# Optimization experiments

Hardware: AMD Instinct MI355X
Metric: run time of the kernel (lower is better)

The kernel has to match this reference:

```python
import jax, jax.numpy as jnp
import numpy as np

B, C, T = 8, 512, 8192
NQ, CBS, CBD = 9, 1024, 8
EPS = 1e-12  # F.normalize eps


def setup_inputs() -> dict:
    key = jax.random.key(0)
    ks = jax.random.split(key, 12)
    n = lambda i, shape, s: jax.random.normal(ks[i], shape, jnp.float32) * s
    return {
        "z": n(0, (B, C, T), 1.0),
        "down_w": n(1, (2, C, C, 2), 0.02),   # [layer, out, in, k] (torch Conv1d layout)
        "down_b": n(2, (2, C), 0.01),
        "up_w": n(3, (2, C, C, 2), 0.02),     # [layer, in, out, k] (torch ConvTranspose1d layout)
        "up_b": n(4, (2, C), 0.01),
        "in_v": n(5, (NQ, CBD, C), 0.05),     # weight_norm direction of in_proj 1x1 conv
        "in_g": 1.0 + n(6, (NQ, CBD), 0.02),  # weight_norm magnitude
        "in_b": n(7, (NQ, CBD), 0.01),
        "out_v": n(8, (NQ, C, CBD), 0.05),
        "out_g": 1.0 + n(9, (NQ, C), 0.02),
        "out_b": n(10, (NQ, C), 0.01),
        "codebooks": n(11, (NQ, CBS, CBD), 1.0),
    }


def _wn(g, v):
    # weight_norm (dim=0): per-output-row rescale
    return g[:, None] * v / jnp.linalg.norm(v, axis=1, keepdims=True)


def _l2norm(x):
    return x / jnp.maximum(jnp.linalg.norm(x, axis=-1, keepdims=True), EPS)


def _forward(z, down_w, down_b, up_w, up_b, in_v, in_g, in_b, out_v, out_g, out_b, codebooks):
    # --- downsample: two Conv1d(k=2, s=2) ---
    x = z
    for l in range(2):
        b, c, t = x.shape
        xr = x.reshape(b, c, t // 2, 2)
        x = jnp.einsum('bitk,oik->bot', xr, down_w[l]) + down_b[l][None, :, None]

    residual = x
    z_q = jnp.zeros_like(x)
    commit_loss = jnp.float32(0.0)
    cb_loss = jnp.float32(0.0)
    codes = []
    for i in range(NQ):
        # in_proj 1x1 conv (weight-normed)
        w_in = _wn(in_g[i], in_v[i])                 # [CBD, C]
        z_e = jnp.einsum('bdt,cd->bct', residual, w_in) + in_b[i][None, :, None]  # [B, CBD, T']
        # decode_latents: L2-normalize + squared-euclid via matmul + argmax
        bt = z_e.shape[0] * z_e.shape[2]
        enc = z_e.transpose(0, 2, 1).reshape(bt, CBD)
        enc_n = _l2norm(enc)
        cbk = codebooks[i]
        cb_n = _l2norm(cbk)
        dist = ((enc_n ** 2).sum(1, keepdims=True)
                - 2.0 * enc_n @ cb_n.T
                + (cb_n ** 2).sum(1)[None, :])        # [B*T', CBS]
        idx = jnp.argmax(-dist, axis=1).reshape(z_e.shape[0], -1)  # [B, T']
        z_q_i = cbk[idx].transpose(0, 2, 1)           # [B, CBD, T'] (un-normalized codebook rows)
        # losses (eval: mask all-true -> per-batch mean over (1,2) then batch mean == global mean)
        commit_loss = commit_loss + ((z_e - jax.lax.stop_gradient(z_q_i)) ** 2).mean()
        cb_loss = cb_loss + ((z_q_i - jax.lax.stop_gradient(z_e)) ** 2).mean()
        # straight-through + out_proj 1x1 conv (weight-normed)
        z_st = z_e + jax.lax.stop_gradient(z_q_i - z_e)
        w_out = _wn(out_g[i], out_v[i])               # [C, CBD]
        z_q_out = jnp.einsum('bct,dc->bdt', z_st, w_out) + out_b[i][None, :, None]
        z_q = z_q + z_q_out
        residual = residual - z_q_out
        codes.append(idx)
    codes = jnp.stack(codes, axis=1)                  # [B, NQ, T']

    x = z_q
    for l in range(2):
        b, c, t = x.shape
        x = jnp.einsum('bit,iok->botk', x, up_w[l]).reshape(b, C, t * 2) + up_b[l][None, :, None]
    return x, codes, commit_loss, cb_loss


def reference(z, down_w, down_b, up_w, up_b, in_v, in_g, in_b, out_v, out_g, out_b, codebooks):
    return _forward(z, down_w, down_b, up_w, up_b, in_v, in_g, in_b, out_v, out_g, out_b, codebooks)
```

## Files before the change

### kernel.cpp

```cpp
#include <hip/hip_runtime.h>
#include <math.h>


using u16 = unsigned short;
typedef __attribute__((ext_vector_type(8))) short bf16x8;
typedef __attribute__((ext_vector_type(8))) u16 su16x8;
typedef __attribute__((ext_vector_type(4))) float f32x4;

constexpr int NQ = 9, CBS = 1024, CBD = 8;
constexpr int TQ = 2048;
constexpr int NTOK = 16384;
constexpr int APS = 1048576;
#define EPSN 1e-12f

constexpr size_t OFF_X2    = 0;
constexpr size_t OFF_E0T   = 8388608;
constexpr size_t OFF_Q     = 9568256;
constexpr size_t OFF_WD    = 10747904;
constexpr size_t OFF_WDP   = 11796480;
constexpr size_t OFF_WEFF  = 13369344;
constexpr size_t OFF_WX    = 14417920;
constexpr size_t OFF_WINN  = 14581760;
constexpr size_t OFF_WOUTS = 14618624;
constexpr size_t OFF_CBS   = 14659584;
constexpr size_t OFF_PT    = 14678016;
constexpr size_t OFF_BEFF  = 14680356;
constexpr size_t OFF_BSUM  = 14680428;
constexpr size_t OFF_BD    = 14680940;
constexpr size_t OFF_BUP   = 14681452;
constexpr size_t OFF_LOSS  = 14682476;

__global__ void prep_small1(const float* __restrict__ in_v, const float* __restrict__ in_g,
                            const float* __restrict__ out_v, const float* __restrict__ out_g,
                            const float* __restrict__ out_b, const float* __restrict__ codebooks,
                            const float* __restrict__ down_w, const float* __restrict__ down_b,
                            const float* __restrict__ up_w, const float* __restrict__ up_b,
                            float* __restrict__ ws) {
  int bid = blockIdx.x, tid = threadIdx.x;
  int wid4 = tid >> 6, lane = tid & 63;
  if (bid < 18) {
    int wid = bid * 4 + wid4;
    if (wid < 72) {
      const float* v = in_v + (size_t)wid * 512;
      float ss = 0.f;
      for (int c = lane; c < 512; c += 64) ss += v[c] * v[c];
      #pragma unroll
      for (int o = 32; o; o >>= 1) ss += __shfl_xor(ss, o);
      float sc = in_g[wid] / sqrtf(ss);
      float* dst = ws + OFF_WINN + (size_t)wid * 512;
      for (int c = lane; c < 512; c += 64) dst[c] = v[c] * sc;
    }
  } else if (bid < 36) {
    int r = (bid - 18) * 256 + tid;
    if (r < 4608) {
      int i = r >> 9, c = r & 511;
      const float* v = out_v + (size_t)r * 8;
      float ss = 0.f;
      #pragma unroll
      for (int d = 0; d < 8; d++) ss += v[d] * v[d];
      float sc = out_g[r] / sqrtf(ss);
      float* dst = ws + OFF_WOUTS + (size_t)c * 80 + i * 8;
      #pragma unroll
      for (int d = 0; d < 8; d++) dst[d] = v[d] * sc;
    }
  } else if (bid < 72) {
    int r = (bid - 36) * 256 + tid;
    if (r < 9216) {
      int i = r >> 10, j = r & 1023;
      const float* v = codebooks + (size_t)r * 8;
      float ss = 0.f;
      #pragma unroll
      for (int d = 0; d < 8; d++) ss += v[d] * v[d];
      float nm = fmaxf(sqrtf(ss), EPSN);
      float nsq = 0.f;
      #pragma unroll
      for (int d = 0; d < 8; d++) { float cn = v[d] / nm; nsq += cn * cn; }
      ws[OFF_CBS + ((size_t)i * 2 + 0) * 1024 + j] = 2.0f / nm;
      ws[OFF_CBS + ((size_t)i * 2 + 1) * 1024 + j] = nsq;
    }
  } else if (bid < 74) {
    int c = (bid - 72) * 256 + tid;
    if (c < 512) {
      float s = 0.f;
      #pragma unroll
      for (int j = 0; j < 9; j++) s += out_b[j * 512 + c];
      ws[OFF_BSUM + c] = s;
      ws[OFF_WOUTS + (size_t)c * 80 + 72] = s;
      #pragma unroll
      for (int d = 73; d < 80; d++) ws[OFF_WOUTS + (size_t)c * 80 + d] = 0.f;
    }
  } else if (bid < 202) {
    int o = (bid - 74) * 4 + wid4;
    float s = 0.f;
    for (int m = lane; m < 512; m += 64) {
      float w0 = down_w[524288 + (size_t)o * 1024 + m * 2];
      float w1 = down_w[524288 + (size_t)o * 1024 + m * 2 + 1];
      s += (w0 + w1) * down_b[m];
    }
    #pragma unroll
    for (int off = 32; off; off >>= 1) s += __shfl_xor(s, off);
    if (lane == 0) ws[OFF_BD + o] = s + down_b[512 + o];
  } else {
    int gw = (bid - 202) * 4 + wid4;
    int c = gw >> 1, j2 = gw & 1;
    float s = 0.f;
    for (int m = lane; m < 512; m += 64)
      s += up_w[524288 + (size_t)m * 1024 + c * 2 + j2] * up_b[m];
    #pragma unroll
    for (int off = 32; off; off >>= 1) s += __shfl_xor(s, off);
    if (lane == 0) ws[OFF_BUP + gw] = s + up_b[512 + c];
  }
}

__global__ void prep2(const float* __restrict__ in_b, const float* __restrict__ out_b,
                      float* __restrict__ ws) {
  int gw = blockIdx.x * 4 + (threadIdx.x >> 6), lane = threadIdx.x & 63;
  const float* WinN = ws + OFF_WINN;
  const float* WoutS = ws + OFF_WOUTS;
  if (gw < 2304) {
    int tri = gw >> 6, dd = gw & 63;
    int ip = 1;
    while (tri >= ip * (ip + 1) / 2) ip++;
    int i = tri - ip * (ip - 1) / 2;
    int d = dd >> 3, dp = dd & 7;
    const float* a = WinN + (size_t)(ip * 8 + d) * 512;
    float s = 0.f;
    for (int c = lane; c < 512; c += 64) s += a[c] * WoutS[(size_t)c * 80 + i * 8 + dp];
    #pragma unroll
    for (int o = 32; o; o >>= 1) s += __shfl_xor(s, o);
    if (lane == 0) ws[OFF_PT + (size_t)tri * 65 + dd] = s;
  } else if (gw < 2376) {
    int r = gw - 2304;
    int i = r >> 3;
    const float* a = WinN + (size_t)r * 512;
    float s = 0.f;
    for (int c = lane; c < 512; c += 64) {
      float ob = 0.f;
      for (int j = 0; j < i; j++) ob += out_b[j * 512 + c];
      s += a[c] * ob;
    }
    #pragma unroll
    for (int o = 32; o; o >>= 1) s += __shfl_xor(s, o);
    if (lane == 0) ws[OFF_BEFF + r] = in_b[r] - s;
  }
}

template <int WHICH>
__global__ __launch_bounds__(256) void smallmm(const float* __restrict__ src,
                                               float* __restrict__ outp) {
  __shared__ float As[32][68];
  __shared__ float Bs[32][68];
  const int tid = threadIdx.x;
  const int tx = tid & 15, ty = tid >> 4;
  const int b0 = blockIdx.x * 64, a0 = blockIdx.y * 64, j = blockIdx.z;
  const int jh = j >> 1, jl = j & 1;
  float acc[4][4];
  #pragma unroll
  for (int i = 0; i < 4; i++)
    #pragma unroll
    for (int k = 0; k < 4; k++) acc[i][k] = 0.f;

  for (int k0 = 0; k0 < 512; k0 += 32) {
    #pragma unroll
    for (int rep = 0; rep < 8; rep++) {
      int f = tid + rep * 256;
      int aa = f >> 5, mm = f & 31;
      size_t ai;
      if constexpr (WHICH == 0) ai = 524288 + (size_t)(a0 + aa) * 1024 + (k0 + mm) * 2 + jh;
      else                      ai = 524288 + (size_t)(k0 + mm) * 1024 + (a0 + aa) * 2 + jl;
      As[mm][aa] = src[ai];
      int mm2 = f >> 6, bb = f & 63;
      size_t bi;
      if constexpr (WHICH == 0) bi = (size_t)(k0 + mm2) * 1024 + (b0 + bb) * 2 + jl;
      else                      bi = (size_t)(b0 + bb) * 1024 + (k0 + mm2) * 2 + jh;
      Bs[mm2][bb] = src[bi];
    }
    __syncthreads();
    #pragma unroll
    for (int kk = 0; kk < 32; kk++) {
      float av[4], bv[4];
      #pragma unroll
      for (int i = 0; i < 4; i++) av[i] = As[kk][ty * 4 + i];
      #pragma unroll
      for (int i = 0; i < 4; i++) bv[i] = Bs[kk][tx * 4 + i];
      #pragma unroll
      for (int i = 0; i < 4; i++)
        #pragma unroll
        for (int k = 0; k < 4; k++) acc[i][k] = fmaf(av[i], bv[k], acc[i][k]);
    }
    __syncthreads();
  }
  #pragma unroll
  for (int i = 0; i < 4; i++) {
    int a = a0 + ty * 4 + i;
    #pragma unroll
    for (int k = 0; k < 4; k++) {
      int b = b0 + tx * 4 + k;
      if constexpr (WHICH == 0) outp[(size_t)a * 2048 + b * 4 + j] = acc[i][k];
      else                      outp[((size_t)a * 4 + j) * 512 + b] = acc[i][k];
    }
  }
}

__global__ void prep_wdsplit(const float* __restrict__ wd, u16* __restrict__ wdp) {
  int idx = blockIdx.x * 256 + threadIdx.x;
  float v = wd[idx];
  unsigned u = __float_as_uint(v);
  wdp[idx] = (u16)(u >> 16);
  float r = v - __uint_as_float(u & 0xFFFF0000u);
  unsigned ur = __float_as_uint(r);
  wdp[APS + idx] = (u16)(ur >> 16);
  float r2 = r - __uint_as_float(ur & 0xFFFF0000u);
  wdp[2 * APS + idx] = (u16)(__float_as_uint(r2) >> 16);
}

__global__ __launch_bounds__(256) void prep_wx(const float* __restrict__ weff,
                                               const float* __restrict__ wouts,
                                               float* __restrict__ wx) {
  __shared__ float Wes[16][512];
  __shared__ float WSs[64][80];
  const int tid = threadIdx.x;
  const int m0 = blockIdx.x * 16;
  #pragma unroll
  for (int rep = 0; rep < 32; rep++) {
    int f = tid + rep * 256;
    Wes[f >> 9][f & 511] = weff[(size_t)(m0 + (f >> 9)) * 512 + (f & 511)];
  }
  const int rowq = tid >> 4, rq = tid & 15;
  float accs[5] = {0.f, 0.f, 0.f, 0.f, 0.f};
  for (int k0 = 0; k0 < 512; k0 += 64) {
    __syncthreads();
    #pragma unroll
    for (int rep = 0; rep < 20; rep++) {
      int f = tid + rep * 256;
      int kk = f / 80, col = f % 80;
      WSs[kk][col] = wouts[(size_t)(k0 + kk) * 80 + col];
    }
    __syncthreads();
    #pragma unroll 4
    for (int kk = 0; kk < 64; kk++) {
      float we = Wes[rowq][k0 + kk];
      #pragma unroll
      for (int s = 0; s < 5; s++) accs[s] = fmaf(we, WSs[kk][rq + 16 * s], accs[s]);
    }
  }
  #pragma unroll
  for (int s = 0; s < 5; s++) {
    int r = rq + 16 * s;
    if (r < 73) wx[(size_t)(m0 + rowq) * 80 + r] = accs[s];
  }
  if (tid < 112) {
    int row = tid / 7, col = 73 + tid % 7;
    wx[(size_t)(m0 + row) * 80 + col] = 0.f;
  }
}

__global__ __launch_bounds__(512) void gemm_down(const u16* __restrict__ Ap,
                                                 const float* __restrict__ z,
                                                 const float* __restrict__ bias,
                                                 float* __restrict__ Out) {
  constexpr int NS = 3, K = 2048;
  __shared__ u16 Bp[2][NS][128][32];
  const int tid = threadIdx.x;
  const int w = tid >> 6, l = tid & 63;
  const int g = l >> 4, li = l & 15;
  const int wr = w >> 2, wc = w & 3;
  const int n0 = blockIdx.x * 128, m0 = blockIdx.y * 128;
  const int nn = tid & 127, kq = tid >> 7;
  const int bb = n0 >> 11;
  const int tb = (n0 & 2047) + nn;

  f32x4 acc[4][2];
  #pragma unroll
  for (int a = 0; a < 4; a++)
    #pragma unroll
    for (int b = 0; b < 2; b++) acc[a][b] = (f32x4){0.f, 0.f, 0.f, 0.f};

  float pvA[8], pvB[8];

#define LOADB(PV, K0)                                                           \
  {                                                                             \
    int c0_ = ((K0) >> 2) + kq * 2;                                             \
    _Pragma("unroll")                                                           \
    for (int cc_ = 0; cc_ < 2; ++cc_)                                           \
      *(float4*)&PV[4 * cc_] =                                                  \
          *(const float4*)(z + ((size_t)(bb * 512 + c0_ + cc_) << 13) + 4 * tb);\
  }

  const int sw = (nn >> 1) & 3;
  const int cw = (kq ^ sw) << 3;

#define STAGE(BUF, PV)                                                          \
  {                                                                             \
    su16x8 pa_[NS];                                                             \
    _Pragma("unroll")                                                           \
    for (int j_ = 0; j_ < 8; ++j_) {                                            \
      float v_ = PV[j_];                                                        \
      unsigned u_ = __float_as_uint(v_);                                        \
      pa_[0][j_] = (u16)(u_ >> 16);                                             \
      float r_ = v_ - __uint_as_float(u_ & 0xFFFF0000u);                        \
      unsigned ur_ = __float_as_uint(r_);                                       \
      pa_[1][j_] = (u16)(ur_ >> 16);                                            \
      float r2_ = r_ - __uint_as_float(ur_ & 0xFFFF0000u);                      \
      pa_[2][j_] = (u16)(__float_as_uint(r2_) >> 16);                           \
    }                                                                           \
    _Pragma("unroll")                                                           \
    for (int p_ = 0; p_ < NS; ++p_)                                             \
      *(su16x8*)&Bp[BUF][p_][nn][cw] = pa_[p_];                                 \
  }

#define COMPUTE(BUF, K0)                                                        \
  {                                                                             \
    bf16x8 bfr_[2][NS];                                                         \
    _Pragma("unroll")                                                           \
    for (int fn_ = 0; fn_ < 2; ++fn_) {                                         \
      int row_ = wc * 32 + fn_ * 16 + li;                                       \
      int cs_ = ((g ^ ((row_ >> 1) & 3)) << 3);                                 \
      _Pragma("unroll")                                                         \
      for (int q_ = 0; q_ < NS; ++q_)                                           \
        bfr_[fn_][q_] = *(const bf16x8*)&Bp[BUF][q_][row_][cs_];                \
    }                                                                           \
    const u16* arow_ = Ap + (size_t)(m0 + wr * 64 + li) * K + (K0) + g * 8;     \
    _Pragma("unroll")                                                           \
    for (int fm_ = 0; fm_ < 4; ++fm_) {                                         \
      bf16x8 afr_[NS];                                                          \
      _Pragma("unroll")                                                         \
      for (int p_ = 0; p_ < NS; ++p_)                                           \
        afr_[p_] = *(const bf16x8*)(arow_ + (size_t)p_ * APS + (size_t)fm_ * 16 * K); \
      _Pragma("unroll")                                                         \
      for (int fn_ = 0; fn_ < 2; ++fn_) {                                       \
        f32x4 a_ = acc[fm_][fn_];                                               \
        a_ = __builtin_amdgcn_mfma_f32_16x16x32_bf16(afr_[2], bfr_[fn_][0], a_, 0, 0, 0); \
        a_ = __builtin_amdgcn_mfma_f32_16x16x32_bf16(afr_[1], bfr_[fn_][1], a_, 0, 0, 0); \
        a_ = __builtin_amdgcn_mfma_f32_16x16x32_bf16(afr_[0], bfr_[fn_][2], a_, 0, 0, 0); \
        a_ = __builtin_amdgcn_mfma_f32_16x16x32_bf16(afr_[1], bfr_[fn_][0], a_, 0, 0, 0); \
        a_ = __builtin_amdgcn_mfma_f32_16x16x32_bf16(afr_[0], bfr_[fn_][1], a_, 0, 0, 0); \
        a_ = __builtin_amdgcn_mfma_f32_16x16x32_bf16(afr_[0], bfr_[fn_][0], a_, 0, 0, 0); \
        acc[fm_][fn_] = a_;                                                     \
      }                                                                         \
    }                                                                           \
  }

  LOADB(pvA, 0)
  LOADB(pvB, 32)
  STAGE(0, pvA)
  LOADB(pvA, 64)
  __syncthreads();

  for (int k0 = 0; k0 < K; k0 += 64) {
    STAGE(1, pvB)
    if (k0 + 96 < K) { LOADB(pvB, k0 + 96) }
    COMPUTE(0, k0)
    __syncthreads();
    if (k0 + 64 < K) { STAGE(0, pvA) }
    if (k0 + 128 < K) { LOADB(pvA, k0 + 128) }
    COMPUTE(1, k0 + 32)
    __syncthreads();
  }
#undef LOADB
#undef STAGE
#undef COMPUTE

  const int mb = m0 + wr * 64 + g * 4;
  const int nb = n0 + wc * 32 + li;
  #pragma unroll
  for (int fn = 0; fn < 2; ++fn) {
    int n = nb + fn * 16;
    int b = n >> 11, t = n & 2047;
    #pragma unroll
    for (int fm = 0; fm < 4; ++fm)
      #pragma unroll
      for (int r = 0; r < 4; ++r) {
        int o = mb + fm * 16 + r;
        Out[((size_t)((b << 9) + o)) * 2048 + t] = acc[fm][fn][r] + bias[o];
      }
  }
}

__global__ __launch_bounds__(256) void gemm_e0f(const float* __restrict__ A,
                                                const float* __restrict__ Bsrc,
                                                float* __restrict__ e0t) {
  constexpr int M = 72, K = 512, Tt = 2048;
  __shared__ float As[16][132];
  __shared__ float Bs[16][68];
  int tid = threadIdx.x;
  int tx = tid & 7, ty = tid >> 3;
  int n0 = blockIdx.x * 64;
  int b = n0 / Tt, t0 = n0 % Tt;
  float acc[4][8];
  #pragma unroll
  for (int i = 0; i < 4; i++)
    #pragma unroll
    for (int j = 0; j < 8; j++) acc[i][j] = 0.f;

  for (int k0 = 0; k0 < K; k0 += 16) {
    #pragma unroll
    for (int rep = 0; rep < 2; rep++) {
      int f = tid + rep * 256;
      int row = f >> 2, c4 = (f & 3) << 2;
      int m = row, k = k0 + c4;
      float4 v = make_float4(0.f, 0.f, 0.f, 0.f);
      if (m < M) v = *(const float4*)(A + (size_t)m * K + k);
      As[c4 + 0][row] = v.x; As[c4 + 1][row] = v.y;
      As[c4 + 2][row] = v.z; As[c4 + 3][row] = v.w;
    }
    {
      int kk = tid >> 4, n4 = (tid & 15) << 2;
      float4 v = *(const float4*)(Bsrc + ((size_t)(b * K + k0 + kk)) * Tt + t0 + n4);
      *(float4*)&Bs[kk][n4] = v;
    }
    __syncthreads();
    #pragma unroll
    for (int kk = 0; kk < 16; kk++) {
      float a[4], bb[8];
      #pragma unroll
      for (int i = 0; i < 4; i++) a[i] = As[kk][ty * 4 + i];
      *(float4*)&bb[0] = *(float4*)&Bs[kk][tx * 8];
      *(float4*)&bb[4] = *(float4*)&Bs[kk][tx * 8 + 4];
      #pragma unroll
      for (int i = 0; i < 4; i++)
        #pragma unroll
        for (int j = 0; j < 8; j++) acc[i][j] = fmaf(a[i], bb[j], acc[i][j]);
    }
    __syncthreads();
  }
  #pragma unroll
  for (int j = 0; j < 8; j++) {
    int n = n0 + tx * 8 + j;
    #pragma unroll
    for (int i = 0; i < 4; i++) {
      int m = ty * 4 + i;
      if (m < M) e0t[(size_t)n * M + m] = acc[i][j];
    }
  }
}

__global__ __launch_bounds__(256) void xfin(const float* __restrict__ wx,
                                            const float* __restrict__ Q,
                                            const float* __restrict__ bup,
                                            float* __restrict__ xout) {
  __shared__ float Wxs[128][80];
  __shared__ float Qs[128][80];
  const int tid = threadIdx.x;
  const int n0 = blockIdx.x * 128, m0 = blockIdx.y * 128;
  #pragma unroll
  for (int rep = 0; rep < 10; rep++) {
    int f = tid + rep * 256;
    *(float4*)&Wxs[0][f * 4] = *(const float4*)(wx + (size_t)m0 * 80 + f * 4);
  }
  {
    int nn = tid & 127, r0 = tid >> 7;
    for (int r = r0; r < 72; r += 2)
      Qs[nn][r] = Q[(size_t)r * 16384 + n0 + nn];
  }
  __syncthreads();

  const int txn = tid & 15, tym = tid >> 4;
  float acc[8][8];
  #pragma unroll
  for (int i = 0; i < 8; i++)
    #pragma unroll
    for (int j = 0; j < 8; j++) acc[i][j] = 0.f;

  #pragma unroll 2
  for (int r4 = 0; r4 < 18; r4++) {
    float4 wv[8], qv[8];
    #pragma unroll
    for (int i = 0; i < 8; i++) wv[i] = *(const float4*)&Wxs[tym * 8 + i][r4 * 4];
    #pragma unroll
    for (int j = 0; j < 8; j++) qv[j] = *(const float4*)&Qs[txn * 8 + j][r4 * 4];
    #pragma unroll
    for (int i = 0; i < 8; i++)
      #pragma unroll
      for (int j = 0; j < 8; j++) {
        acc[i][j] = fmaf(wv[i].x, qv[j].x, acc[i][j]);
        acc[i][j] = fmaf(wv[i].y, qv[j].y, acc[i][j]);
        acc[i][j] = fmaf(wv[i].z, qv[j].z, acc[i][j]);
        acc[i][j] = fmaf(wv[i].w, qv[j].w, acc[i][j]);
      }
  }

  float bxv[8];
  #pragma unroll
  for (int mi = 0; mi < 8; mi++) {
    int mp = m0 + tym * 8 + mi;
    bxv[mi] = Wxs[tym * 8 + mi][72] + bup[(mp >> 2) * 2 + (mp & 1)];
  }
  #pragma unroll
  for (int cg = 0; cg < 2; cg++) {
    int mp0 = m0 + tym * 8 + cg * 4;
    int c = mp0 >> 2;
    #pragma unroll
    for (int j = 0; j < 8; j++) {
      int n = n0 + txn * 8 + j;
      int b = n >> 11, t = n & 2047;
      float4 sv = make_float4(acc[cg * 4 + 0][j] + bxv[cg * 4 + 0],
                              acc[cg * 4 + 1][j] + bxv[cg * 4 + 1],
                              acc[cg * 4 + 2][j] + bxv[cg * 4 + 2],
                              acc[cg * 4 + 3][j] + bxv[cg * 4 + 3]);
      *(float4*)&xout[((size_t)((b << 9) + c)) * 8192 + 4 * t] = sv;
    }
  }
}

__global__ __launch_bounds__(256) void rvq_kernel(const float* __restrict__ codebooks,
                                                  const float* __restrict__ e0t,
                                                  const float* __restrict__ cbsW,
                                                  const float* __restrict__ ptW,
                                                  const float* __restrict__ beffW,
                                                  float* __restrict__ Qout,
                                                  float* __restrict__ codesOut,
                                                  float* __restrict__ lossPart) {
  __shared__ float cbv[8][1024];
  __shared__ float cbs2[2][1024];
  __shared__ float Pt[36 * 65];
  __shared__ float est[16][72];
  __shared__ float lred[4];
  int tid = threadIdx.x, wid = tid >> 6, lane = tid & 63;
  int nb0 = blockIdx.x * 16;
  for (int idx = tid; idx < 2340; idx += 256) Pt[idx] = ptW[idx];
  for (int idx = tid; idx < 16 * 72; idx += 256)
    est[idx / 72][idx % 72] = e0t[(size_t)nb0 * 72 + idx] + beffW[idx % 72];
  float lossLocal = 0.f;

  for (int i = 0; i < NQ; i++) {
    __syncthreads();
    const float* cbg = codebooks + (size_t)i * CBS * CBD;
    for (int lin = tid; lin < 2048; lin += 256) {
      int j = lin >> 1, half = (lin & 1) << 2;
      float4 v = *(const float4*)(cbg + (size_t)j * 8 + half);
      cbv[half + 0][j] = v.x; cbv[half + 1][j] = v.y;
      cbv[half + 2][j] = v.z; cbv[half + 3][j] = v.w;
    }
    for (int lin = tid; lin < 1024; lin += 256) {
      cbs2[0][lin] = cbsW[((size_t)i * 2 + 0) * 1024 + lin];
      cbs2[1][lin] = cbsW[((size_t)i * 2 + 1) * 1024 + lin];
    }
    __syncthreads();

    float ze[4][8], en[4][8];
    #pragma unroll
    for (int w = 0; w < 4; w++) {
      int tokl = wid * 4 + w;
      float ss = 0.f;
      #pragma unroll
      for (int d = 0; d < 8; d++) { float v = est[tokl][i * 8 + d]; ze[w][d] = v; ss += v * v; }
      float inv = 1.0f / fmaxf(sqrtf(ss), EPSN);
      #pragma unroll
      for (int d = 0; d < 8; d++) en[w][d] = ze[w][d] * inv;
    }
    float best[4]; int bidx[4];
    #pragma unroll
    for (int w = 0; w < 4; w++) { best[w] = -INFINITY; bidx[w] = 0; }
    #pragma unroll 4
    for (int r = 0; r < 16; r++) {
      int j = lane + (r << 6);
      float c0 = cbv[0][j], c1 = cbv[1][j], c2 = cbv[2][j], c3 = cbv[3][j];
      float c4 = cbv[4][j], c5 = cbv[5][j], c6 = cbv[6][j], c7 = cbv[7][j];
      float ti = cbs2[0][j], ns = cbs2[1][j];
      #pragma unroll
      for (int w = 0; w < 4; w++) {
        float dt = en[w][0] * c0;
        dt = fmaf(en[w][1], c1, dt); dt = fmaf(en[w][2], c2, dt);
        dt = fmaf(en[w][3], c3, dt); dt = fmaf(en[w][4], c4, dt);
        dt = fmaf(en[w][5], c5, dt); dt = fmaf(en[w][6], c6, dt);
        dt = fmaf(en[w][7], c7, dt);
        float s = fmaf(dt, ti, -ns);
        if (s > best[w]) { best[w] = s; bidx[w] = j; }
      }
    }
    #pragma unroll
    for (int w = 0; w < 4; w++) {
      #pragma unroll
      for (int off = 32; off; off >>= 1) {
        float so = __shfl_xor(best[w], off);
        int jo = __shfl_xor(bidx[w], off);
        if (so > best[w] || (so == best[w] && jo < bidx[w])) { best[w] = so; bidx[w] = jo; }
      }
    }
    int d = lane & 7;
    #pragma unroll
    for (int w = 0; w < 4; w++) {
      int jstar = bidx[w];
      int tokl = wid * 4 + w;
      int n = nb0 + tokl;
      float qd = cbv[d][jstar];
      float diff = ze[w][d] - qd;
      float sq = diff * diff;
      sq += __shfl_xor(sq, 1); sq += __shfl_xor(sq, 2); sq += __shfl_xor(sq, 4);
      if (lane == 0) lossLocal += sq;
      if (lane < 8) Qout[(size_t)(i * 8 + lane) * NTOK + n] = qd;
      if (lane == 0) codesOut[(size_t)((n >> 11) * NQ + i) * TQ + (n & (TQ - 1))] = (float)jstar;
      if (i < NQ - 1) {
        int f = lane >> 3, d2 = lane & 7;
        int ip = i + 1 + f;
        if (ip < NQ) {
          int tri = (ip * (ip - 1)) / 2 + i;
          const float* prow = &Pt[tri * 65 + d2 * 8];
          float s = 0.f;
          #pragma unroll
          for (int dp = 0; dp < 8; dp++) s = fmaf(prow[dp], cbv[dp][jstar], s);
          est[tokl][ip * 8 + d2] -= s;
        }
      }
    }
  }
  if (lane == 0) lred[wid] = lossLocal;
  __syncthreads();
  if (tid == 0) {
    float s = ((lred[0] + lred[1]) + lred[2]) + lred[3];
    lossPart[blockIdx.x] = s;
  }
}

__global__ void loss_fin(const float* __restrict__ lossPart, float* __restrict__ out) {
  __shared__ float s[256];
  int tid = threadIdx.x;
  float v = 0.f;
  for (int r = 0; r < 4; r++) v += lossPart[tid + r * 256];
  s[tid] = v;
  __syncthreads();
  for (int w = 128; w; w >>= 1) {
    if (tid < w) s[tid] += s[tid + w];
    __syncthreads();
  }
  if (tid == 0) {
    float total = s[0] / 131072.0f;
    out[0] = total;
    out[1] = total;
  }
}

extern "C" void kernel_launch(void* const* d_in, const int* in_sizes, int n_in,
                              void* d_out, int out_size, void* d_ws, size_t ws_size,
                              hipStream_t stream) {
  const float* z      = (const float*)d_in[0];
  const float* down_w = (const float*)d_in[1];
  const float* down_b = (const float*)d_in[2];
  const float* up_w   = (const float*)d_in[3];
  const float* up_b   = (const float*)d_in[4];
  const float* in_v   = (const float*)d_in[5];
  const float* in_g   = (const float*)d_in[6];
  const float* in_b   = (const float*)d_in[7];
  const float* out_v  = (const float*)d_in[8];
  const float* out_g  = (const float*)d_in[9];
  const float* out_b  = (const float*)d_in[10];
  const float* codebooks = (const float*)d_in[11];
  float* ws = (float*)d_ws;
  float* xout = (float*)d_out;
  float* codesOut = xout + (size_t)8 * 512 * 8192;
  float* lossOut = codesOut + (size_t)8 * NQ * TQ;

  hipLaunchKernelGGL(prep_small1, dim3(458), dim3(256), 0, stream,
                     in_v, in_g, out_v, out_g, out_b, codebooks,
                     down_w, down_b, up_w, up_b, ws);
  hipLaunchKernelGGL(prep2, dim3(594), dim3(256), 0, stream, in_b, out_b, ws);
  hipLaunchKernelGGL((smallmm<0>), dim3(8, 8, 4), dim3(256), 0, stream, down_w, ws + OFF_WD);
  hipLaunchKernelGGL((smallmm<1>), dim3(8, 8, 4), dim3(256), 0, stream, up_w, ws + OFF_WEFF);
  hipLaunchKernelGGL(prep_wdsplit, dim3(4096), dim3(256), 0, stream,
                     ws + OFF_WD, (u16*)(ws + OFF_WDP));
  hipLaunchKernelGGL(prep_wx, dim3(128), dim3(256), 0, stream,
                     ws + OFF_WEFF, ws + OFF_WOUTS, ws + OFF_WX);
  hipLaunchKernelGGL(gemm_down, dim3(128, 4), dim3(512), 0, stream,
                     (const u16*)(ws + OFF_WDP), z, ws + OFF_BD, ws + OFF_X2);
  hipLaunchKernelGGL(gemm_e0f, dim3(256), dim3(256), 0, stream,
                     ws + OFF_WINN, ws + OFF_X2, ws + OFF_E0T);
  hipLaunchKernelGGL(rvq_kernel, dim3(1024), dim3(256), 0, stream,
                     codebooks, ws + OFF_E0T, ws + OFF_CBS, ws + OFF_PT, ws + OFF_BEFF,
                     ws + OFF_Q, codesOut, ws + OFF_LOSS);
  hipLaunchKernelGGL(xfin, dim3(128, 16), dim3(256), 0, stream,
                     ws + OFF_WX, ws + OFF_Q, ws + OFF_BUP, xout);
  hipLaunchKernelGGL(loss_fin, dim3(1), dim3(256), 0, stream, ws + OFF_LOSS, lossOut);
}
```

Baseline: 935.9 us.

## Use 4-wave 64x64 warp tiles in gemm_down and prefetch A fragments

The gemm_down block drops from 8 waves to 4, so each wave now computes a 64x64 output tile instead of 64x32. Each B fragment read from LDS is therefore reused across more MFMAs. Each thread also loads twice as much of z per stage. The A-matrix fragments for the next K step are now register double-buffered (afrA/afrB) and loaded from global memory one step ahead, rather than at compute time. The cost is much higher register pressure (16 accumulators plus 24 A fragments) and fewer waves per block to hide latency.

Measured after the change: 813.6 us. -13.1%, faster.

```diff
diff --git a/kernel.cpp b/kernel.cpp
--- a/kernel.cpp
+++ b/kernel.cpp
@@ -255,7 +255,7 @@
   }
 }
 
-__global__ __launch_bounds__(512) void gemm_down(const u16* __restrict__ Ap,
+__global__ __launch_bounds__(256) void gemm_down(const u16* __restrict__ Ap,
                                                  const float* __restrict__ z,
                                                  const float* __restrict__ bias,
                                                  float* __restrict__ Out) {
@@ -264,78 +264,96 @@
   const int tid = threadIdx.x;
   const int w = tid >> 6, l = tid & 63;
   const int g = l >> 4, li = l & 15;
-  const int wr = w >> 2, wc = w & 3;
+  const int wr = w >> 1, wc = w & 1;
   const int n0 = blockIdx.x * 128, m0 = blockIdx.y * 128;
-  const int nn = tid & 127, kq = tid >> 7;
+  const int nn = tid & 127, kw = tid >> 7;
   const int bb = n0 >> 11;
   const int tb = (n0 & 2047) + nn;
 
-  f32x4 acc[4][2];
+  f32x4 acc[4][4];
   #pragma unroll
   for (int a = 0; a < 4; a++)
     #pragma unroll
-    for (int b = 0; b < 2; b++) acc[a][b] = (f32x4){0.f, 0.f, 0.f, 0.f};
-
-  float pvA[8], pvB[8];
+    for (int b = 0; b < 4; b++) acc[a][b] = (f32x4){0.f, 0.f, 0.f, 0.f};
+
+  float pvA[16], pvB[16];
+  bf16x8 afrA[4][NS], afrB[4][NS];
+  const u16* arow = Ap + (size_t)(m0 + wr * 64 + li) * K + g * 8;
 
 #define LOADB(PV, K0)                                                           \
   {                                                                             \
-    int c0_ = ((K0) >> 2) + kq * 2;                                             \
+    int c0_ = ((K0) >> 2) + kw * 4;                                             \
     _Pragma("unroll")                                                           \
-    for (int cc_ = 0; cc_ < 2; ++cc_)                                           \
+    for (int cc_ = 0; cc_ < 4; ++cc_)                                           \
       *(float4*)&PV[4 * cc_] =                                                  \
           *(const float4*)(z + ((size_t)(bb * 512 + c0_ + cc_) << 13) + 4 * tb);\
   }
 
+#define LOADA(DST, K0)                                                          \
+  {                                                                             \
+    _Pragma("unroll")                                                           \
+    for (int fm_ = 0; fm_ < 4; ++fm_)                                           \
+      _Pragma("unroll")                                                         \
+      for (int p_ = 0; p_ < NS; ++p_)                                           \
+        DST[fm_][p_] = *(const bf16x8*)(arow + (size_t)p_ * APS +               \
+                                        (size_t)fm_ * 16 * K + (K0));           \
+  }
+
   const int sw = (nn >> 1) & 3;
-  const int cw = (kq ^ sw) << 3;
+  const int c0 = ((2 * kw) ^ sw) << 3, c1 = ((2 * kw + 1) ^ sw) << 3;
 
 #define STAGE(BUF, PV)                                                          \
   {                                                                             \
-    su16x8 pa_[NS];                                                             \
+    su16x8 pa_[NS], pb_[NS];                                                    \
     _Pragma("unroll")                                                           \
     for (int j_ = 0; j_ < 8; ++j_) {                                            \
-      float v_ = PV[j_];                                                        \
-      unsigned u_ = __float_as_uint(v_);                                        \
-      pa_[0][j_] = (u16)(u_ >> 16);                                             \
-      float r_ = v_ - __uint_as_float(u_ & 0xFFFF0000u);                        \
-      unsigned ur_ = __float_as_uint(r_);                                       \
-      pa_[1][j_] = (u16)(ur_ >> 16);                                            \
-      float r2_ = r_ - __uint_as_float(ur_ & 0xFFFF0000u);                      \
-      pa_[2][j_] = (u16)(__float_as_uint(r2_) >> 16);                           \
+      {                                                                         \
+        float v_ = PV[j_];                                                      \
+        unsigned u_ = __float_as_uint(v_);                                      \
+        pa_[0][j_] = (u16)(u_ >> 16);                                           \
+        float r_ = v_ - __uint_as_float(u_ & 0xFFFF0000u);                      \
+        unsigned ur_ = __float_as_uint(r_);                                     \
+        pa_[1][j_] = (u16)(ur_ >> 16);                                          \
+        float r2_ = r_ - __uint_as_float(ur_ & 0xFFFF0000u);                    \
+        pa_[2][j_] = (u16)(__float_as_uint(r2_) >> 16);                         \
+      }                                                                         \
+      {                                                                         \
+        float v_ = PV[8 + j_];                                                  \
+        unsigned u_ = __float_as_uint(v_);                                      \
+        pb_[0][j_] = (u16)(u_ >> 16);                                           \
+        float r_ = v_ - __uint_as_float(u_ & 0xFFFF0000u);                      \
+        unsigned ur_ = __float_as_uint(r_);                                     \
+        pb_[1][j_] = (u16)(ur_ >> 16);                                          \
+        float r2_ = r_ - __uint_as_float(ur_ & 0xFFFF0000u);                    \
+        pb_[2][j_] = (u16)(__float_as_uint(r2_) >> 16);                         \
+      }                                                                         \
     }                                                                           \
     _Pragma("unroll")                                                           \
-    for (int p_ = 0; p_ < NS; ++p_)                                             \
-      *(su16x8*)&Bp[BUF][p_][nn][cw] = pa_[p_];                                 \
-  }
-
-#define COMPUTE(BUF, K0)                                                        \
+    for (int p_ = 0; p_ < NS; ++p_) {                                           \
+      *(su16x8*)&Bp[BUF][p_][nn][c0] = pa_[p_];                                 \
+      *(su16x8*)&Bp[BUF][p_][nn][c1] = pb_[p_];                                 \
+    }                                                                           \
+  }
+
+#define COMPUTE(BUF, AFR)                                                       \
   {                                                                             \
-    bf16x8 bfr_[2][NS];                                                         \
     _Pragma("unroll")                                                           \
-    for (int fn_ = 0; fn_ < 2; ++fn_) {                                         \
-      int row_ = wc * 32 + fn_ * 16 + li;                                       \
+    for (int fn_ = 0; fn_ < 4; ++fn_) {                                         \
+      int row_ = wc * 64 + fn_ * 16 + li;                                       \
       int cs_ = ((g ^ ((row_ >> 1) & 3)) << 3);                                 \
+      bf16x8 bfr_[NS];                                                          \
       _Pragma("unroll")                                                         \
       for (int q_ = 0; q_ < NS; ++q_)                                           \
-        bfr_[fn_][q_] = *(const bf16x8*)&Bp[BUF][q_][row_][cs_];                \
-    }                                                                           \
-    const u16* arow_ = Ap + (size_t)(m0 + wr * 64 + li) * K + (K0) + g * 8;     \
-    _Pragma("unroll")                                                           \
-    for (int fm_ = 0; fm_ < 4; ++fm_) {                                         \
-      bf16x8 afr_[NS];                                                          \
+        bfr_[q_] = *(const bf16x8*)&Bp[BUF][q_][row_][cs_];                     \
       _Pragma("unroll")                                                         \
-      for (int p_ = 0; p_ < NS; ++p_)                                           \
-        afr_[p_] = *(const bf16x8*)(arow_ + (size_t)p_ * APS + (size_t)fm_ * 16 * K); \
-      _Pragma("unroll")                                                         \
-      for (int fn_ = 0; fn_ < 2; ++fn_) {                                       \
+      for (int fm_ = 0; fm_ < 4; ++fm_) {                                       \
         f32x4 a_ = acc[fm_][fn_];                                               \
-        a_ = __builtin_amdgcn_mfma_f32_16x16x32_bf16(afr_[2], bfr_[fn_][0], a_, 0, 0, 0); \
-        a_ = __builtin_amdgcn_mfma_f32_16x16x32_bf16(afr_[1], bfr_[fn_][1], a_, 0, 0, 0); \
-        a_ = __builtin_amdgcn_mfma_f32_16x16x32_bf16(afr_[0], bfr_[fn_][2], a_, 0, 0, 0); \
-        a_ = __builtin_amdgcn_mfma_f32_16x16x32_bf16(afr_[1], bfr_[fn_][0], a_, 0, 0, 0); \
-        a_ = __builtin_amdgcn_mfma_f32_16x16x32_bf16(afr_[0], bfr_[fn_][1], a_, 0, 0, 0); \
-        a_ = __builtin_amdgcn_mfma_f32_16x16x32_bf16(afr_[0], bfr_[fn_][0], a_, 0, 0, 0); \
+        a_ = __builtin_amdgcn_mfma_f32_16x16x32_bf16(AFR[fm_][2], bfr_[0], a_, 0, 0, 0); \
+        a_ = __builtin_amdgcn_mfma_f32_16x16x32_bf16(AFR[fm_][1], bfr_[1], a_, 0, 0, 0); \
+        a_ = __builtin_amdgcn_mfma_f32_16x16x32_bf16(AFR[fm_][0], bfr_[2], a_, 0, 0, 0); \
+        a_ = __builtin_amdgcn_mfma_f32_16x16x32_bf16(AFR[fm_][1], bfr_[0], a_, 0, 0, 0); \
+        a_ = __builtin_amdgcn_mfma_f32_16x16x32_bf16(AFR[fm_][0], bfr_[1], a_, 0, 0, 0); \
+        a_ = __builtin_amdgcn_mfma_f32_16x16x32_bf16(AFR[fm_][0], bfr_[0], a_, 0, 0, 0); \
         acc[fm_][fn_] = a_;                                                     \
       }                                                                         \
     }                                                                           \
@@ -345,26 +363,30 @@
   LOADB(pvB, 32)
   STAGE(0, pvA)
   LOADB(pvA, 64)
+  LOADA(afrA, 0)
   __syncthreads();
 
   for (int k0 = 0; k0 < K; k0 += 64) {
     STAGE(1, pvB)
     if (k0 + 96 < K) { LOADB(pvB, k0 + 96) }
-    COMPUTE(0, k0)
+    LOADA(afrB, k0 + 32)
+    COMPUTE(0, afrA)
     __syncthreads();
     if (k0 + 64 < K) { STAGE(0, pvA) }
     if (k0 + 128 < K) { LOADB(pvA, k0 + 128) }
-    COMPUTE(1, k0 + 32)
+    if (k0 + 64 < K) { LOADA(afrA, k0 + 64) }
+    COMPUTE(1, afrB)
     __syncthreads();
   }
 #undef LOADB
+#undef LOADA
 #undef STAGE
 #undef COMPUTE
 
   const int mb = m0 + wr * 64 + g * 4;
-  const int nb = n0 + wc * 32 + li;
-  #pragma unroll
-  for (int fn = 0; fn < 2; ++fn) {
+  const int nb = n0 + wc * 64 + li;
+  #pragma unroll
+  for (int fn = 0; fn < 4; ++fn) {
     int n = nb + fn * 16;
     int b = n >> 11, t = n & 2047;
     #pragma unroll
@@ -661,7 +683,7 @@
                      ws + OFF_WD, (u16*)(ws + OFF_WDP));
   hipLaunchKernelGGL(prep_wx, dim3(128), dim3(256), 0, stream,
                      ws + OFF_WEFF, ws + OFF_WOUTS, ws + OFF_WX);
-  hipLaunchKernelGGL(gemm_down, dim3(128, 4), dim3(512), 0, stream,
+  hipLaunchKernelGGL(gemm_down, dim3(128, 4), dim3(256), 0, stream,
                      (const u16*)(ws + OFF_WDP), z, ws + OFF_BD, ws + OFF_X2);
   hipLaunchKernelGGL(gemm_e0f, dim3(256), dim3(256), 0, stream,
                      ws + OFF_WINN, ws + OFF_X2, ws + OFF_E0T);
```
